# Kernel optimization log

Hardware: AMD Instinct MI355X
Metric: run time of the kernel (lower is better)

## Reference

```python
import jax, jax.numpy as jnp
import numpy as np

IN_DIM = 512
OUT_DIM = 512


def setup_inputs() -> dict:
    key = jax.random.key(0)
    ks = jax.random.split(key, 7)
    B, S = 4, 2048
    scale = 1.0 / np.sqrt(IN_DIM)
    X = jax.random.normal(ks[0], (B, S, IN_DIM), dtype=jnp.float32)
    Wq = jax.random.normal(ks[1], (IN_DIM, OUT_DIM), dtype=jnp.float32) * scale
    Wk = jax.random.normal(ks[2], (IN_DIM, OUT_DIM), dtype=jnp.float32) * scale
    Wv = jax.random.normal(ks[3], (IN_DIM, OUT_DIM), dtype=jnp.float32) * scale
    bq = jnp.zeros((OUT_DIM,), dtype=jnp.float32)
    bk = jnp.zeros((OUT_DIM,), dtype=jnp.float32)
    bv = jnp.zeros((OUT_DIM,), dtype=jnp.float32)
    return {"X": X, "Wq": Wq, "bq": bq, "Wk": Wk, "bk": bk, "Wv": Wv, "bv": bv}


def reference(X, Wq, bq, Wk, bk, Wv, bv):
    # Q/K/V projections: [B,S,in] @ [in,out] -> [B,S,out]
    Q = X @ Wq + bq
    K = X @ Wk + bk
    V = X @ Wv + bv
    d_k = jnp.asarray(Q.shape[-1], Q.dtype)
    # scores: [B,S,S] = QK^T / sqrt(d_k)
    scores = jnp.einsum('bsd,btd->bst', Q, K) / jnp.sqrt(d_k)
    attn = jax.nn.softmax(scores, axis=-1)
    # out: [B,S,out]
    return jnp.einsum('bst,btd->bsd', attn, V)
```

## Files before the change

kernel.cpp:

```cpp
#include <hip/hip_runtime.h>
#include <hip/hip_bf16.h>
#include <stdint.h>

#define SEQ   2048
#define DIM   512
#define BATCH 4

typedef __attribute__((ext_vector_type(8))) short  short8;
typedef __attribute__((ext_vector_type(4))) float  floatx4;

static __device__ __forceinline__ unsigned short f2b(float f) {
  return __builtin_bit_cast(unsigned short, __float2bfloat16(f));
}


template<int AM, int AN, int KIT, int TKA, int TKB>
__device__ __forceinline__ void fgemm(
    const short8* __restrict__ A, int rt0A,
    const short8* __restrict__ B, int rt0B,
    int lane, floatx4 (&acc)[AM][AN])
{
  short8 af0[AM], bf0[AN], af1[AM], bf1[AN];
#pragma unroll
  for (int q = 0; q < AM; ++q) af0[q] = A[((rt0A + q) * TKA + 0) * 64 + lane];
#pragma unroll
  for (int q = 0; q < AN; ++q) bf0[q] = B[((rt0B + q) * TKB + 0) * 64 + lane];

  for (int kt = 0; kt < KIT; kt += 2) {
#pragma unroll
    for (int q = 0; q < AM; ++q) af1[q] = A[((rt0A + q) * TKA + kt + 1) * 64 + lane];
#pragma unroll
    for (int q = 0; q < AN; ++q) bf1[q] = B[((rt0B + q) * TKB + kt + 1) * 64 + lane];
#pragma unroll
    for (int i = 0; i < AM; ++i)
#pragma unroll
      for (int j = 0; j < AN; ++j)
        acc[i][j] = __builtin_amdgcn_mfma_f32_16x16x32_bf16(af0[i], bf0[j], acc[i][j], 0, 0, 0);
    if (kt + 2 < KIT) {
#pragma unroll
      for (int q = 0; q < AM; ++q) af0[q] = A[((rt0A + q) * TKA + kt + 2) * 64 + lane];
#pragma unroll
      for (int q = 0; q < AN; ++q) bf0[q] = B[((rt0B + q) * TKB + kt + 2) * 64 + lane];
    }
#pragma unroll
    for (int i = 0; i < AM; ++i)
#pragma unroll
      for (int j = 0; j < AN; ++j)
        acc[i][j] = __builtin_amdgcn_mfma_f32_16x16x32_bf16(af1[i], bf1[j], acc[i][j], 0, 0, 0);
  }
}

__global__ __launch_bounds__(256) void convx_kernel(
    const float* __restrict__ X, short8* __restrict__ XbF)
{
  const int flat = blockIdx.x * 256 + threadIdx.x;
  const int tile = flat >> 6, lane = flat & 63;
  const int row = (tile >> 4) * 16 + (lane & 15);
  const int k0  = (tile & 15) * 32 + (lane >> 4) * 8;
  const float4 v0 = *(const float4*)(X + (size_t)row * DIM + k0);
  const float4 v1 = *(const float4*)(X + (size_t)row * DIM + k0 + 4);
  short8 o;
  o[0] = (short)f2b(v0.x); o[1] = (short)f2b(v0.y);
  o[2] = (short)f2b(v0.z); o[3] = (short)f2b(v0.w);
  o[4] = (short)f2b(v1.x); o[5] = (short)f2b(v1.y);
  o[6] = (short)f2b(v1.z); o[7] = (short)f2b(v1.w);
  XbF[flat] = o;
}

__global__ __launch_bounds__(256) void convw_kernel(
    const float* __restrict__ Wq, const float* __restrict__ Wk,
    const float* __restrict__ Wv, short8* __restrict__ WF)
{
  const int z = blockIdx.y;
  const float* W = (z == 0) ? Wq : (z == 1) ? Wk : Wv;
  const int flat = blockIdx.x * 256 + threadIdx.x;
  const int tile = flat >> 6, lane = flat & 63;
  const int n  = (tile >> 4) * 16 + (lane & 15);
  const int k0 = (tile & 15) * 32 + (lane >> 4) * 8;
  short8 o;
#pragma unroll
  for (int e = 0; e < 8; ++e)
    o[e] = (short)f2b(W[(size_t)(k0 + e) * DIM + n]);
  WF[z * 32768 + flat] = o;
}

__global__ __launch_bounds__(256) void zfill_kernel(float4* __restrict__ p)
{
  p[blockIdx.x * 256 + threadIdx.x] = float4{0.f, 0.f, 0.f, 0.f};
}

__global__ __launch_bounds__(256) void qkv_kernel(
    const short8* __restrict__ XbF, const short8* __restrict__ WF,
    const float* __restrict__ bq, const float* __restrict__ bk, const float* __restrict__ bv,
    unsigned short* __restrict__ QF, unsigned short* __restrict__ KF,
    unsigned short* __restrict__ VF)
{
  const int z = blockIdx.z;
  const int lane = threadIdx.x & 63, wid = threadIdx.x >> 6;
  const int wm = wid & 1, wn = wid >> 1;
  floatx4 acc[4][4] = {};

  if (z < 2) {
    fgemm<4, 4, 16, 16, 16>(WF + z * 32768, blockIdx.y * 8 + wm * 4,
                            XbF, blockIdx.x * 8 + wn * 4, lane, acc);
    const float* bias = z ? bk : bq;
    unsigned short* OF = z ? KF : QF;
    const int db = blockIdx.y * 128 + wm * 64, sb = blockIdx.x * 128 + wn * 64;
#pragma unroll
    for (int i = 0; i < 4; ++i) {
      const int d0 = db + i * 16 + (lane >> 4) * 4;
      const float4 b4 = *(const float4*)(bias + d0);
#pragma unroll
      for (int j = 0; j < 4; ++j) {
        const int s = sb + j * 16 + (lane & 15);
        ushort4 pk;
        pk.x = f2b(acc[i][j][0] + b4.x);
        pk.y = f2b(acc[i][j][1] + b4.y);
        pk.z = f2b(acc[i][j][2] + b4.z);
        pk.w = f2b(acc[i][j][3] + b4.w);
        *(ushort4*)(OF + (size_t)((s >> 4) * 16 + (d0 >> 5)) * 512 +
                    ((((d0 & 31) >> 3) << 4) | (s & 15)) * 8 + (d0 & 7)) = pk;
      }
    }
  } else {
    fgemm<4, 4, 16, 16, 16>(XbF, blockIdx.x * 8 + wm * 4,
                            WF + 2 * 32768, blockIdx.y * 8 + wn * 4, lane, acc);
    const int sbb = blockIdx.x * 128 + wm * 64, db = blockIdx.y * 128 + wn * 64;
#pragma unroll
    for (int i = 0; i < 4; ++i) {
      const int s0 = sbb + i * 16 + (lane >> 4) * 4;
      const int bt = s0 >> 11, t0 = s0 & 2047;
#pragma unroll
      for (int j = 0; j < 4; ++j) {
        const int d = db + j * 16 + (lane & 15);
        const float bn = bv[d];
        ushort4 pk;
        pk.x = f2b(acc[i][j][0] + bn);
        pk.y = f2b(acc[i][j][1] + bn);
        pk.z = f2b(acc[i][j][2] + bn);
        pk.w = f2b(acc[i][j][3] + bn);
        *(ushort4*)(VF + (size_t)bt * DIM * SEQ +
                    (size_t)((d >> 4) * 64 + (t0 >> 5)) * 512 +
                    ((((t0 & 31) >> 3) << 4) | (d & 15)) * 8 + (t0 & 7)) = pk;
      }
    }
  }
}

__global__ __launch_bounds__(256) void scT_kernel(
    const short8* __restrict__ QF, const short8* __restrict__ KF,
    unsigned short* __restrict__ ScF, float* __restrict__ rowsum)
{
  const int b = blockIdx.z;
  const int lane = threadIdx.x & 63, wid = threadIdx.x >> 6;
  const int wm = wid & 1, wn = wid >> 1;
  floatx4 acc[4][4] = {};
  fgemm<4, 4, 16, 16, 16>(KF + (size_t)b * 131072, blockIdx.y * 8 + wm * 4,
                          QF + (size_t)b * 131072, blockIdx.x * 8 + wn * 4, lane, acc);

  unsigned short* S = ScF + (size_t)b * SEQ * SEQ;
  const float scale = 0.044194173824159216f;
  const int tb = blockIdx.y * 128 + wm * 64, sb = blockIdx.x * 128 + wn * 64;
  float colsum[4] = {0.f, 0.f, 0.f, 0.f};
#pragma unroll
  for (int i = 0; i < 4; ++i) {
    const int t0 = tb + i * 16 + (lane >> 4) * 4;
#pragma unroll
    for (int j = 0; j < 4; ++j) {
      const int s = sb + j * 16 + (lane & 15);
      float e0 = __expf(acc[i][j][0] * scale);
      float e1 = __expf(acc[i][j][1] * scale);
      float e2 = __expf(acc[i][j][2] * scale);
      float e3 = __expf(acc[i][j][3] * scale);
      colsum[j] += (e0 + e1) + (e2 + e3);
      ushort4 pk;
      pk.x = f2b(e0); pk.y = f2b(e1); pk.z = f2b(e2); pk.w = f2b(e3);
      *(ushort4*)(S + (size_t)((s >> 4) * 64 + (t0 >> 5)) * 512 +
                  ((((t0 & 31) >> 3) << 4) | (s & 15)) * 8 + (t0 & 7)) = pk;
    }
  }
#pragma unroll
  for (int j = 0; j < 4; ++j) {
    colsum[j] += __shfl_xor(colsum[j], 16, 64);
    colsum[j] += __shfl_xor(colsum[j], 32, 64);
  }
  if ((lane >> 4) == 0) {
#pragma unroll
    for (int j = 0; j < 4; ++j)
      atomicAdd(rowsum + b * SEQ + sb + j * 16 + lane, colsum[j]);
  }
}

__global__ __launch_bounds__(256) void pv_kernel(
    const short8* __restrict__ ScF, const short8* __restrict__ VF,
    const float* __restrict__ rowsum, float* __restrict__ out)
{
  const int b = blockIdx.z;
  const int lane = threadIdx.x & 63, wid = threadIdx.x >> 6;
  floatx4 acc[2][4] = {};
  fgemm<2, 4, 64, 64, 64>(ScF + (size_t)b * 524288, blockIdx.x * 8 + wid * 2,
                          VF + (size_t)b * 131072, blockIdx.y * 4, lane, acc);

  const int mb = blockIdx.x * 128 + wid * 32, db = blockIdx.y * 64;
#pragma unroll
  for (int i = 0; i < 2; ++i) {
    const int m0 = mb + i * 16 + (lane >> 4) * 4;
    const float4 rs = *(const float4*)(rowsum + b * SEQ + m0);
    const float inv0 = 1.f / rs.x, inv1 = 1.f / rs.y, inv2 = 1.f / rs.z, inv3 = 1.f / rs.w;
#pragma unroll
    for (int j = 0; j < 4; ++j) {
      const int d = db + j * 16 + (lane & 15);
      float* o = out + ((size_t)b * SEQ + m0) * DIM + d;
      o[0 * DIM] = acc[i][j][0] * inv0;
      o[1 * DIM] = acc[i][j][1] * inv1;
      o[2 * DIM] = acc[i][j][2] * inv2;
      o[3 * DIM] = acc[i][j][3] * inv3;
    }
  }
}

extern "C" void kernel_launch(void* const* d_in, const int* in_sizes, int n_in,
                              void* d_out, int out_size, void* d_ws, size_t ws_size,
                              hipStream_t stream) {
  const float* X  = (const float*)d_in[0];
  const float* Wq = (const float*)d_in[1];
  const float* bq = (const float*)d_in[2];
  const float* Wk = (const float*)d_in[3];
  const float* bk = (const float*)d_in[4];
  const float* Wv = (const float*)d_in[5];
  const float* bv = (const float*)d_in[6];
  float* out = (float*)d_out;
  char* ws = (char*)d_ws;

  short8* XbF = (short8*)(ws + 0);
  float*  rowsum = (float*)(ws + 0);
  short8* WF  = (short8*)(ws + 8388608);
  char*   QF  = ws + 9961472;
  char*   KF  = ws + 18350080;
  char*   VF  = ws + 26738688;
  char*   ScF = ws + 35127296;

  convx_kernel<<<dim3(2048), 256, 0, stream>>>(X, XbF);
  convw_kernel<<<dim3(128, 3), 256, 0, stream>>>(Wq, Wk, Wv, WF);
  qkv_kernel<<<dim3(64, 4, 3), 256, 0, stream>>>(
      XbF, WF, bq, bk, bv,
      (unsigned short*)QF, (unsigned short*)KF, (unsigned short*)VF);
  zfill_kernel<<<dim3(8), 256, 0, stream>>>((float4*)rowsum);
  scT_kernel<<<dim3(16, 16, 4), 256, 0, stream>>>(
      (const short8*)QF, (const short8*)KF, (unsigned short*)ScF, rowsum);
  pv_kernel<<<dim3(16, 8, 4), 256, 0, stream>>>(
      (const short8*)ScF, (const short8*)VF, rowsum, out);
}
```

Baseline: 159.8 us.

## Stage GEMM operands through double-buffered LDS and merge setup kernels

Replaces the register-only fragment GEMM, where each wave read its own fragments straight from global memory, with a block-shared LDS GEMM. Tiles are staged with global_load_lds into a double buffer, so the waves of a block share A/B tiles instead of re-reading them. The X/W conversion and rowsum zero-fill kernels are merged into one setup kernel, which removes two launches, and rowsum moves to its own workspace region. The PV kernel's wave tiling changes to 4x2 fragments per wave, and the new path adds a __syncthreads per k-step.

```diff
diff --git a/kernel.cpp b/kernel.cpp
--- a/kernel.cpp
+++ b/kernel.cpp
@@ -13,106 +13,130 @@
   return __builtin_bit_cast(unsigned short, __float2bfloat16(f));
 }
 
-
-template<int AM, int AN, int KIT, int TKA, int TKB>
-__device__ __forceinline__ void fgemm(
-    const short8* __restrict__ A, int rt0A,
-    const short8* __restrict__ B, int rt0B,
-    int lane, floatx4 (&acc)[AM][AN])
-{
-  short8 af0[AM], bf0[AN], af1[AM], bf1[AN];
-#pragma unroll
-  for (int q = 0; q < AM; ++q) af0[q] = A[((rt0A + q) * TKA + 0) * 64 + lane];
-#pragma unroll
-  for (int q = 0; q < AN; ++q) bf0[q] = B[((rt0B + q) * TKB + 0) * 64 + lane];
-
-  for (int kt = 0; kt < KIT; kt += 2) {
-#pragma unroll
-    for (int q = 0; q < AM; ++q) af1[q] = A[((rt0A + q) * TKA + kt + 1) * 64 + lane];
-#pragma unroll
-    for (int q = 0; q < AN; ++q) bf1[q] = B[((rt0B + q) * TKB + kt + 1) * 64 + lane];
-#pragma unroll
-    for (int i = 0; i < AM; ++i)
-#pragma unroll
-      for (int j = 0; j < AN; ++j)
-        acc[i][j] = __builtin_amdgcn_mfma_f32_16x16x32_bf16(af0[i], bf0[j], acc[i][j], 0, 0, 0);
-    if (kt + 2 < KIT) {
-#pragma unroll
-      for (int q = 0; q < AM; ++q) af0[q] = A[((rt0A + q) * TKA + kt + 2) * 64 + lane];
-#pragma unroll
-      for (int q = 0; q < AN; ++q) bf0[q] = B[((rt0B + q) * TKB + kt + 2) * 64 + lane];
-    }
-#pragma unroll
-    for (int i = 0; i < AM; ++i)
-#pragma unroll
-      for (int j = 0; j < AN; ++j)
-        acc[i][j] = __builtin_amdgcn_mfma_f32_16x16x32_bf16(af1[i], bf1[j], acc[i][j], 0, 0, 0);
-  }
-}
-
-__global__ __launch_bounds__(256) void convx_kernel(
-    const float* __restrict__ X, short8* __restrict__ XbF)
+static __device__ __forceinline__ void gll16(const void* g, void* l) {
+  __builtin_amdgcn_global_load_lds(
+      (__attribute__((address_space(1))) void*)(uintptr_t)g,
+      (__attribute__((address_space(3))) void*)l, 16, 0, 0);
+}
+
+
+template <int BF>
+__device__ __forceinline__ void fgemm_lds(
+    const char* __restrict__ A, int rtA0, int TKA,
+    const char* __restrict__ B, int rtB0, int TKB,
+    int kIters, char* lds, floatx4 (&acc)[4][BF / 2])
+{
+  constexpr int BUF = (8 + BF) * 1024;
+  const int tid = threadIdx.x;
+  const int w = tid >> 6, l = tid & 63;
+  const int wmf = (w & 1) * 4;
+  const int wnf = (w >> 1) * (BF / 2);
+
+  auto stage = [&](int p, int kt) {
+    char* dst = lds + p * BUF;
+#pragma unroll
+    for (int q = 0; q < 2; ++q) {
+      const int f = q * 4 + w;
+      gll16(A + (((size_t)(rtA0 + f) * TKA + kt) << 10) + l * 16,
+            dst + f * 1024 + l * 16);
+    }
+#pragma unroll
+    for (int q = 0; q < BF / 4; ++q) {
+      const int f = q * 4 + w;
+      gll16(B + (((size_t)(rtB0 + f) * TKB + kt) << 10) + l * 16,
+            dst + 8192 + f * 1024 + l * 16);
+    }
+  };
+
+  stage(0, 0);
+  __syncthreads();
+
+  for (int kt = 0; kt < kIters; ++kt) {
+    const int p = kt & 1;
+    if (kt + 1 < kIters) stage(1 - p, kt + 1);
+
+    const char* bA = lds + p * BUF;
+    const char* bB = bA + 8192;
+    short8 af[4], bf[BF / 2];
+#pragma unroll
+    for (int i = 0; i < 4; ++i)
+      af[i] = *(const short8*)(bA + (wmf + i) * 1024 + l * 16);
+#pragma unroll
+    for (int j = 0; j < BF / 2; ++j)
+      bf[j] = *(const short8*)(bB + (wnf + j) * 1024 + l * 16);
+
+#pragma unroll
+    for (int i = 0; i < 4; ++i)
+#pragma unroll
+      for (int j = 0; j < BF / 2; ++j)
+        acc[i][j] = __builtin_amdgcn_mfma_f32_16x16x32_bf16(af[i], bf[j], acc[i][j], 0, 0, 0);
+
+    __syncthreads();
+  }
+}
+
+__global__ __launch_bounds__(256) void setup_kernel(
+    const float* __restrict__ X, const float* __restrict__ Wq,
+    const float* __restrict__ Wk, const float* __restrict__ Wv,
+    short8* __restrict__ XbF, short8* __restrict__ WF,
+    float* __restrict__ rowsum)
 {
   const int flat = blockIdx.x * 256 + threadIdx.x;
-  const int tile = flat >> 6, lane = flat & 63;
-  const int row = (tile >> 4) * 16 + (lane & 15);
-  const int k0  = (tile & 15) * 32 + (lane >> 4) * 8;
-  const float4 v0 = *(const float4*)(X + (size_t)row * DIM + k0);
-  const float4 v1 = *(const float4*)(X + (size_t)row * DIM + k0 + 4);
-  short8 o;
-  o[0] = (short)f2b(v0.x); o[1] = (short)f2b(v0.y);
-  o[2] = (short)f2b(v0.z); o[3] = (short)f2b(v0.w);
-  o[4] = (short)f2b(v1.x); o[5] = (short)f2b(v1.y);
-  o[6] = (short)f2b(v1.z); o[7] = (short)f2b(v1.w);
-  XbF[flat] = o;
-}
-
-__global__ __launch_bounds__(256) void convw_kernel(
-    const float* __restrict__ Wq, const float* __restrict__ Wk,
-    const float* __restrict__ Wv, short8* __restrict__ WF)
-{
-  const int z = blockIdx.y;
-  const float* W = (z == 0) ? Wq : (z == 1) ? Wk : Wv;
-  const int flat = blockIdx.x * 256 + threadIdx.x;
-  const int tile = flat >> 6, lane = flat & 63;
-  const int n  = (tile >> 4) * 16 + (lane & 15);
-  const int k0 = (tile & 15) * 32 + (lane >> 4) * 8;
-  short8 o;
-#pragma unroll
-  for (int e = 0; e < 8; ++e)
-    o[e] = (short)f2b(W[(size_t)(k0 + e) * DIM + n]);
-  WF[z * 32768 + flat] = o;
-}
-
-__global__ __launch_bounds__(256) void zfill_kernel(float4* __restrict__ p)
-{
-  p[blockIdx.x * 256 + threadIdx.x] = float4{0.f, 0.f, 0.f, 0.f};
+  {
+    const int tile = flat >> 6, l = flat & 63;
+    const int row = (tile >> 4) * 16 + (l & 15);
+    const int k0  = (tile & 15) * 32 + (l >> 4) * 8;
+    const float4 v0 = *(const float4*)(X + (size_t)row * DIM + k0);
+    const float4 v1 = *(const float4*)(X + (size_t)row * DIM + k0 + 4);
+    short8 o;
+    o[0] = (short)f2b(v0.x); o[1] = (short)f2b(v0.y);
+    o[2] = (short)f2b(v0.z); o[3] = (short)f2b(v0.w);
+    o[4] = (short)f2b(v1.x); o[5] = (short)f2b(v1.y);
+    o[6] = (short)f2b(v1.z); o[7] = (short)f2b(v1.w);
+    XbF[flat] = o;
+  }
+  if (flat < 3 * 32768) {
+    const int z = flat >> 15, within = flat & 32767;
+    const float* W = (z == 0) ? Wq : (z == 1) ? Wk : Wv;
+    const int tile = within >> 6, l = within & 63;
+    const int n  = (tile >> 4) * 16 + (l & 15);
+    const int k0 = (tile & 15) * 32 + (l >> 4) * 8;
+    short8 o;
+#pragma unroll
+    for (int e = 0; e < 8; ++e)
+      o[e] = (short)f2b(W[(size_t)(k0 + e) * DIM + n]);
+    WF[flat] = o;
+  }
+  if (flat < 2048) ((float4*)rowsum)[flat] = float4{0.f, 0.f, 0.f, 0.f};
 }
 
 __global__ __launch_bounds__(256) void qkv_kernel(
     const short8* __restrict__ XbF, const short8* __restrict__ WF,
-    const float* __restrict__ bq, const float* __restrict__ bk, const float* __restrict__ bv,
+    const float* __restrict__ bq, const float* __restrict__ bk,
+    const float* __restrict__ bv,
     unsigned short* __restrict__ QF, unsigned short* __restrict__ KF,
     unsigned short* __restrict__ VF)
 {
-  const int z = blockIdx.z;
-  const int lane = threadIdx.x & 63, wid = threadIdx.x >> 6;
-  const int wm = wid & 1, wn = wid >> 1;
+  __shared__ char lds[32768];
+  const int z = blockIdx.z, x = blockIdx.x, y = blockIdx.y;
+  const int lane = threadIdx.x & 63, w = threadIdx.x >> 6;
+  const char* Xc = (const char*)XbF;
+  const char* Wc = (const char*)WF;
   floatx4 acc[4][4] = {};
 
   if (z < 2) {
-    fgemm<4, 4, 16, 16, 16>(WF + z * 32768, blockIdx.y * 8 + wm * 4,
-                            XbF, blockIdx.x * 8 + wn * 4, lane, acc);
+    fgemm_lds<8>(Wc + (size_t)z * 524288, y * 8, 16, Xc, x * 8, 16, 16, lds, acc);
     const float* bias = z ? bk : bq;
     unsigned short* OF = z ? KF : QF;
-    const int db = blockIdx.y * 128 + wm * 64, sb = blockIdx.x * 128 + wn * 64;
+    const int dbase = y * 128 + (w & 1) * 64;
+    const int sbase = x * 128 + (w >> 1) * 64;
 #pragma unroll
     for (int i = 0; i < 4; ++i) {
-      const int d0 = db + i * 16 + (lane >> 4) * 4;
+      const int d0 = dbase + i * 16 + (lane >> 4) * 4;
       const float4 b4 = *(const float4*)(bias + d0);
 #pragma unroll
       for (int j = 0; j < 4; ++j) {
-        const int s = sb + j * 16 + (lane & 15);
+        const int s = sbase + j * 16 + (lane & 15);
         ushort4 pk;
         pk.x = f2b(acc[i][j][0] + b4.x);
         pk.y = f2b(acc[i][j][1] + b4.y);
@@ -123,16 +147,16 @@
       }
     }
   } else {
-    fgemm<4, 4, 16, 16, 16>(XbF, blockIdx.x * 8 + wm * 4,
-                            WF + 2 * 32768, blockIdx.y * 8 + wn * 4, lane, acc);
-    const int sbb = blockIdx.x * 128 + wm * 64, db = blockIdx.y * 128 + wn * 64;
+    fgemm_lds<8>(Xc, x * 8, 16, Wc + 2 * 524288, y * 8, 16, 16, lds, acc);
+    const int sbase = x * 128 + (w & 1) * 64;
+    const int dbase = y * 128 + (w >> 1) * 64;
 #pragma unroll
     for (int i = 0; i < 4; ++i) {
-      const int s0 = sbb + i * 16 + (lane >> 4) * 4;
+      const int s0 = sbase + i * 16 + (lane >> 4) * 4;
       const int bt = s0 >> 11, t0 = s0 & 2047;
 #pragma unroll
       for (int j = 0; j < 4; ++j) {
-        const int d = db + j * 16 + (lane & 15);
+        const int d = dbase + j * 16 + (lane & 15);
         const float bn = bv[d];
         ushort4 pk;
         pk.x = f2b(acc[i][j][0] + bn);
@@ -147,20 +171,21 @@
   }
 }
 
-__global__ __launch_bounds__(256) void scT_kernel(
-    const short8* __restrict__ QF, const short8* __restrict__ KF,
+__global__ __launch_bounds__(256) void scores_kernel(
+    const unsigned short* __restrict__ QF, const unsigned short* __restrict__ KF,
     unsigned short* __restrict__ ScF, float* __restrict__ rowsum)
 {
-  const int b = blockIdx.z;
-  const int lane = threadIdx.x & 63, wid = threadIdx.x >> 6;
-  const int wm = wid & 1, wn = wid >> 1;
+  __shared__ char lds[32768];
+  const int b = blockIdx.z, x = blockIdx.x, y = blockIdx.y;
+  const int lane = threadIdx.x & 63, w = threadIdx.x >> 6;
   floatx4 acc[4][4] = {};
-  fgemm<4, 4, 16, 16, 16>(KF + (size_t)b * 131072, blockIdx.y * 8 + wm * 4,
-                          QF + (size_t)b * 131072, blockIdx.x * 8 + wn * 4, lane, acc);
+  fgemm_lds<8>((const char*)KF + (size_t)b * 2097152, y * 8, 16,
+               (const char*)QF + (size_t)b * 2097152, x * 8, 16, 16, lds, acc);
 
   unsigned short* S = ScF + (size_t)b * SEQ * SEQ;
   const float scale = 0.044194173824159216f;
-  const int tb = blockIdx.y * 128 + wm * 64, sb = blockIdx.x * 128 + wn * 64;
+  const int tb = y * 128 + (w & 1) * 64;
+  const int sb = x * 128 + (w >> 1) * 64;
   float colsum[4] = {0.f, 0.f, 0.f, 0.f};
 #pragma unroll
   for (int i = 0; i < 4; ++i) {
@@ -184,7 +209,7 @@
     colsum[j] += __shfl_xor(colsum[j], 16, 64);
     colsum[j] += __shfl_xor(colsum[j], 32, 64);
   }
-  if ((lane >> 4) == 0) {
+  if (lane < 16) {
 #pragma unroll
     for (int j = 0; j < 4; ++j)
       atomicAdd(rowsum + b * SEQ + sb + j * 16 + lane, colsum[j]);
@@ -192,24 +217,24 @@
 }
 
 __global__ __launch_bounds__(256) void pv_kernel(
-    const short8* __restrict__ ScF, const short8* __restrict__ VF,
+    const unsigned short* __restrict__ ScF, const unsigned short* __restrict__ VF,
     const float* __restrict__ rowsum, float* __restrict__ out)
 {
-  const int b = blockIdx.z;
-  const int lane = threadIdx.x & 63, wid = threadIdx.x >> 6;
-  floatx4 acc[2][4] = {};
-  fgemm<2, 4, 64, 64, 64>(ScF + (size_t)b * 524288, blockIdx.x * 8 + wid * 2,
-                          VF + (size_t)b * 131072, blockIdx.y * 4, lane, acc);
-
-  const int mb = blockIdx.x * 128 + wid * 32, db = blockIdx.y * 64;
-#pragma unroll
-  for (int i = 0; i < 2; ++i) {
-    const int m0 = mb + i * 16 + (lane >> 4) * 4;
+  __shared__ char lds[24576];
+  const int b = blockIdx.z, x = blockIdx.x, y = blockIdx.y;
+  const int lane = threadIdx.x & 63, w = threadIdx.x >> 6;
+  floatx4 acc[4][2] = {};
+  fgemm_lds<4>((const char*)ScF + (size_t)b * 8388608, x * 8, 64,
+               (const char*)VF + (size_t)b * 2097152, y * 4, 64, 64, lds, acc);
+
+#pragma unroll
+  for (int i = 0; i < 4; ++i) {
+    const int m0 = x * 128 + (w & 1) * 64 + i * 16 + (lane >> 4) * 4;
     const float4 rs = *(const float4*)(rowsum + b * SEQ + m0);
     const float inv0 = 1.f / rs.x, inv1 = 1.f / rs.y, inv2 = 1.f / rs.z, inv3 = 1.f / rs.w;
 #pragma unroll
-    for (int j = 0; j < 4; ++j) {
-      const int d = db + j * 16 + (lane & 15);
+    for (int j = 0; j < 2; ++j) {
+      const int d = y * 64 + (w >> 1) * 32 + j * 16 + (lane & 15);
       float* o = out + ((size_t)b * SEQ + m0) * DIM + d;
       o[0 * DIM] = acc[i][j][0] * inv0;
       o[1 * DIM] = acc[i][j][1] * inv1;
@@ -233,21 +258,20 @@
   char* ws = (char*)d_ws;
 
   short8* XbF = (short8*)(ws + 0);
-  float*  rowsum = (float*)(ws + 0);
   short8* WF  = (short8*)(ws + 8388608);
   char*   QF  = ws + 9961472;
   char*   KF  = ws + 18350080;
   char*   VF  = ws + 26738688;
   char*   ScF = ws + 35127296;
-
-  convx_kernel<<<dim3(2048), 256, 0, stream>>>(X, XbF);
-  convw_kernel<<<dim3(128, 3), 256, 0, stream>>>(Wq, Wk, Wv, WF);
+  float*  rowsum = (float*)(ws + 68681728);
+
+  setup_kernel<<<dim3(2048), 256, 0, stream>>>(X, Wq, Wk, Wv, XbF, WF, rowsum);
   qkv_kernel<<<dim3(64, 4, 3), 256, 0, stream>>>(
       XbF, WF, bq, bk, bv,
       (unsigned short*)QF, (unsigned short*)KF, (unsigned short*)VF);
-  zfill_kernel<<<dim3(8), 256, 0, stream>>>((float4*)rowsum);
-  scT_kernel<<<dim3(16, 16, 4), 256, 0, stream>>>(
-      (const short8*)QF, (const short8*)KF, (unsigned short*)ScF, rowsum);
+  scores_kernel<<<dim3(16, 16, 4), 256, 0, stream>>>(
+      (const unsigned short*)QF, (const unsigned short*)KF,
+      (unsigned short*)ScF, rowsum);
   pv_kernel<<<dim3(16, 8, 4), 256, 0, stream>>>(
-      (const short8*)ScF, (const short8*)VF, rowsum, out);
-}
+      (const unsigned short*)ScF, (const unsigned short*)VF, rowsum, out);
+}
```

Measured after the change: 150.4 us. 1.06x faster.
